# Optimization experiments

Hardware: AMD Instinct MI355X
Metric: run time of the kernel (lower is better)

The kernel has to match this reference:

```python
import jax, jax.numpy as jnp
import numpy as np

N_NODES = 100000
N_EDGES = 1600000
IN_DIM = 128
HID = 96
N_CLASSES = 16
BN_EPS = 1e-5
GIN_EPS = 0.0  # DGL GINConv default init_eps=0, learn_eps=False


def setup_inputs() -> dict:
    key = jax.random.key(0)
    ks = jax.random.split(key, 16)
    d = {}
    d["h"] = jax.random.normal(ks[0], (N_NODES, IN_DIM), dtype=jnp.float32)
    d["src"] = jax.random.randint(ks[1], (N_EDGES,), 0, N_NODES, dtype=jnp.int32)
    d["dst"] = jax.random.randint(ks[2], (N_EDGES,), 0, N_NODES, dtype=jnp.int32)
    # embedding_h: Linear(input_dim, hidden)
    d["W_emb"] = jax.random.normal(ks[3], (IN_DIM, HID), dtype=jnp.float32) / np.sqrt(IN_DIM)
    d["b_emb"] = jnp.zeros((HID,), dtype=jnp.float32)
    # GIN layer 1: MLP(1 layer) Linear(hid,hid) + BN(hid)
    d["W1"] = jax.random.normal(ks[4], (HID, HID), dtype=jnp.float32) / np.sqrt(HID)
    d["b1"] = jnp.zeros((HID,), dtype=jnp.float32)
    d["g1"] = jnp.ones((HID,), dtype=jnp.float32)
    d["be1"] = jnp.zeros((HID,), dtype=jnp.float32)
    # GIN layer 2
    d["W2"] = jax.random.normal(ks[5], (HID, HID), dtype=jnp.float32) / np.sqrt(HID)
    d["b2"] = jnp.zeros((HID,), dtype=jnp.float32)
    d["g2"] = jnp.ones((HID,), dtype=jnp.float32)
    d["be2"] = jnp.zeros((HID,), dtype=jnp.float32)
    # readout: Linear(hid, n_classes)
    d["Wr"] = jax.random.normal(ks[6], (HID, N_CLASSES), dtype=jnp.float32) / np.sqrt(HID)
    d["br"] = jnp.zeros((N_CLASSES,), dtype=jnp.float32)
    return d


def _gin_layer(h, src, dst, W, b, gamma, beta):
    # sum aggregation over incoming edges: agg[v] = sum_{(u,v) in E} h[u]
    agg = jax.ops.segment_sum(h[src], dst, num_segments=N_NODES)
    z = ((1.0 + GIN_EPS) * h + agg) @ W + b           # MLP (single linear)
    mu = jnp.mean(z, axis=0)                            # BatchNorm1d (batch stats)
    var = jnp.var(z, axis=0)
    z = (z - mu) * jax.lax.rsqrt(var + BN_EPS) * gamma + beta
    return jax.nn.relu(z)


def reference(h, src, dst, W_emb, b_emb, W1, b1, g1, be1, W2, b2, g2, be2, Wr, br):
    h = h @ W_emb + b_emb                               # embedding_h
    h = _gin_layer(h, src, dst, W1, b1, g1, be1)        # dropout treated as identity (eval)
    h = _gin_layer(h, src, dst, W2, b2, g2, be2)
    logits = h @ Wr + br                                # readout
    return jax.nn.log_softmax(logits, axis=1)
```

## Files before the change

### kernel.cpp

```cpp
#include <hip/hip_runtime.h>
#include <cmath>

#define N_NODES 100000
#define N_EDGES 1600000
#define IN_DIM 128
#define HID 96
#define NCLS 16
#define NB_GATH 2048

#define BSHIFT 7
#define BNODES 128
#define NBUK 782
#define TILE_E 8192
#define NBLK_E 196
#define NBLK_Q 24
#define NBLK_R 4

typedef unsigned int uint;
typedef unsigned short ushort;

__device__ __forceinline__ ushort f2bf(float x) {
    uint b = __float_as_uint(x);
    uint r = (b + 0x7FFFu + ((b >> 16) & 1u)) >> 16;
    return (ushort)r;
}
__device__ __forceinline__ float bf2f(ushort u) {
    return __uint_as_float(((uint)u) << 16);
}
__device__ __forceinline__ float bf_lo(uint w) { return __uint_as_float(w << 16); }
__device__ __forceinline__ float bf_hi(uint w) { return __uint_as_float(w & 0xFFFF0000u); }
__device__ __forceinline__ uint pack2bf(float a, float b) {
    return (uint)f2bf(a) | ((uint)f2bf(b) << 16);
}
__device__ __forceinline__ float4 bn_relu4(float4 x, float4 sc, float4 sh) {
    float4 r;
    r.x = fmaxf(fmaf(x.x, sc.x, sh.x), 0.f);
    r.y = fmaxf(fmaf(x.y, sc.y, sh.y), 0.f);
    r.z = fmaxf(fmaf(x.z, sc.z, sh.z), 0.f);
    r.w = fmaxf(fmaf(x.w, sc.w, sh.w), 0.f);
    return r;
}

__device__ __forceinline__ int tile_of(int blk) {
    int xcd = blk & 7, slot = blk >> 3;
    return (xcd < NBLK_R) ? xcd * (NBLK_Q + 1) + slot
                          : NBLK_R * (NBLK_Q + 1) + (xcd - NBLK_R) * NBLK_Q + slot;
}

__global__ __launch_bounds__(256) void wfuse(const float* __restrict__ W_emb,
                                             const float* __restrict__ W1,
                                             const float* __restrict__ b_emb,
                                             float* __restrict__ Wf,
                                             float* __restrict__ bf) {
    __shared__ float W1s[HID * HID];
    for (int i = threadIdx.x; i < HID * HID / 4; i += 256)
        ((float4*)W1s)[i] = ((const float4*)W1)[i];
    __syncthreads();
    int idx = blockIdx.x * 256 + threadIdx.x;
    if (idx < IN_DIM * HID) {
        int i = idx / HID, j = idx - (idx / HID) * HID;
        float acc = 0.f;
        for (int k = 0; k < HID; ++k)
            acc = fmaf(W_emb[(size_t)i * HID + k], W1s[k * HID + j], acc);
        Wf[idx] = acc;
    }
    if (idx < HID) {
        float acc = 0.f;
        for (int k = 0; k < HID; ++k)
            acc = fmaf(b_emb[k], W1s[k * HID + idx], acc);
        bf[idx] = acc;
    }
}

__global__ __launch_bounds__(192) void gemm_l1(const float* __restrict__ X,
                                               const float* __restrict__ W,
                                               const float* __restrict__ bias,
                                               ushort* __restrict__ outB) {
    constexpr int K = IN_DIM, KP = 64;
    constexpr int GSTRIDE = KP * 16 + 4;
    __shared__ float Ws[6 * GSTRIDE];
    __shared__ float bs[HID];
    if (threadIdx.x < HID) bs[threadIdx.x] = bias[threadIdx.x];

    const int g = threadIdx.x % 6;
    const int rc = threadIdx.x / 6;
    const int rbase = blockIdx.x * 64 + rc * 2;
    const int r0 = min(rbase + 0, N_NODES - 1);
    const int r1 = min(rbase + 1, N_NODES - 1);
    const float* x0 = X + (size_t)r0 * K;
    const float* x1 = X + (size_t)r1 * K;
    const float* wg = Ws + g * GSTRIDE;

    float acc[2][16];
#pragma unroll
    for (int j = 0; j < 16; ++j) { acc[0][j] = 0.f; acc[1][j] = 0.f; }

    for (int ph = 0; ph < K / KP; ++ph) {
        if (ph) __syncthreads();
        for (int i = threadIdx.x; i < KP * HID / 4; i += 192) {
            int flat = i * 4;
            int k = flat / HID, c = flat - k * HID;
            int gg = c / 16, j = c - gg * 16;
            *(float4*)&Ws[gg * GSTRIDE + k * 16 + j] =
                *(const float4*)(W + (size_t)(ph * KP + k) * HID + c);
        }
        __syncthreads();
        const float* xp0 = x0 + ph * KP;
        const float* xp1 = x1 + ph * KP;
        for (int k = 0; k < KP; k += 4) {
            float4 a0 = *(const float4*)(xp0 + k);
            float4 a1 = *(const float4*)(xp1 + k);
#pragma unroll
            for (int kk = 0; kk < 4; ++kk) {
                const float* wrow = wg + (k + kk) * 16;
                float4 w0 = *(const float4*)(wrow + 0);
                float4 w1 = *(const float4*)(wrow + 4);
                float4 w2 = *(const float4*)(wrow + 8);
                float4 w3 = *(const float4*)(wrow + 12);
                float xs0 = kk == 0 ? a0.x : kk == 1 ? a0.y : kk == 2 ? a0.z : a0.w;
                float xs1 = kk == 0 ? a1.x : kk == 1 ? a1.y : kk == 2 ? a1.z : a1.w;
                const float wv[16] = {w0.x, w0.y, w0.z, w0.w, w1.x, w1.y, w1.z, w1.w,
                                      w2.x, w2.y, w2.z, w2.w, w3.x, w3.y, w3.z, w3.w};
#pragma unroll
                for (int j = 0; j < 16; ++j) {
                    acc[0][j] = fmaf(xs0, wv[j], acc[0][j]);
                    acc[1][j] = fmaf(xs1, wv[j], acc[1][j]);
                }
            }
        }
    }
    const int rr[2] = {r0, r1};
#pragma unroll
    for (int i = 0; i < 2; ++i) {
        const float* bb = &bs[g * 16];
        ushort* orow = outB + (size_t)rr[i] * HID + g * 16;
        uint4 p0, p1;
        p0.x = pack2bf(acc[i][0] + bb[0], acc[i][1] + bb[1]);
        p0.y = pack2bf(acc[i][2] + bb[2], acc[i][3] + bb[3]);
        p0.z = pack2bf(acc[i][4] + bb[4], acc[i][5] + bb[5]);
        p0.w = pack2bf(acc[i][6] + bb[6], acc[i][7] + bb[7]);
        p1.x = pack2bf(acc[i][8] + bb[8], acc[i][9] + bb[9]);
        p1.y = pack2bf(acc[i][10] + bb[10], acc[i][11] + bb[11]);
        p1.z = pack2bf(acc[i][12] + bb[12], acc[i][13] + bb[13]);
        p1.w = pack2bf(acc[i][14] + bb[14], acc[i][15] + bb[15]);
        *(uint4*)(orow + 0) = p0;
        *(uint4*)(orow + 8) = p1;
    }
}

__global__ __launch_bounds__(192) void gemm_l2(const ushort* __restrict__ X,
                                               const float* __restrict__ W,
                                               const float* __restrict__ scale,
                                               const float* __restrict__ shift,
                                               ushort* __restrict__ outB) {
    constexpr int K = HID, KP = 48;
    constexpr int GSTRIDE = KP * 16 + 4;
    __shared__ float Ws[6 * GSTRIDE];
    __shared__ float scs[HID], shs[HID];
    if (threadIdx.x < HID) {
        scs[threadIdx.x] = scale[threadIdx.x];
        shs[threadIdx.x] = shift[threadIdx.x];
    }

    const int g = threadIdx.x % 6;
    const int rc = threadIdx.x / 6;
    const int rbase = blockIdx.x * 64 + rc * 2;
    const int r0 = min(rbase + 0, N_NODES - 1);
    const int r1 = min(rbase + 1, N_NODES - 1);
    const ushort* x0 = X + (size_t)r0 * K;
    const ushort* x1 = X + (size_t)r1 * K;
    const float* wg = Ws + g * GSTRIDE;

    float acc[2][16];
#pragma unroll
    for (int j = 0; j < 16; ++j) { acc[0][j] = 0.f; acc[1][j] = 0.f; }

    for (int ph = 0; ph < K / KP; ++ph) {
        if (ph) __syncthreads();
        for (int i = threadIdx.x; i < KP * HID / 4; i += 192) {
            int flat = i * 4;
            int k = flat / HID, c = flat - k * HID;
            int gg = c / 16, j = c - gg * 16;
            *(float4*)&Ws[gg * GSTRIDE + k * 16 + j] =
                *(const float4*)(W + (size_t)(ph * KP + k) * HID + c);
        }
        __syncthreads();
        const ushort* xp0 = x0 + ph * KP;
        const ushort* xp1 = x1 + ph * KP;
        for (int k = 0; k < KP; k += 4) {
            uint2 u0 = *(const uint2*)(xp0 + k);
            uint2 u1 = *(const uint2*)(xp1 + k);
            float4 sc4 = *(const float4*)(scs + ph * KP + k);
            float4 sh4 = *(const float4*)(shs + ph * KP + k);
            float4 a0 = bn_relu4(make_float4(bf_lo(u0.x), bf_hi(u0.x), bf_lo(u0.y), bf_hi(u0.y)), sc4, sh4);
            float4 a1 = bn_relu4(make_float4(bf_lo(u1.x), bf_hi(u1.x), bf_lo(u1.y), bf_hi(u1.y)), sc4, sh4);
#pragma unroll
            for (int kk = 0; kk < 4; ++kk) {
                const float* wrow = wg + (k + kk) * 16;
                float4 w0 = *(const float4*)(wrow + 0);
                float4 w1 = *(const float4*)(wrow + 4);
                float4 w2 = *(const float4*)(wrow + 8);
                float4 w3 = *(const float4*)(wrow + 12);
                float xs0 = kk == 0 ? a0.x : kk == 1 ? a0.y : kk == 2 ? a0.z : a0.w;
                float xs1 = kk == 0 ? a1.x : kk == 1 ? a1.y : kk == 2 ? a1.z : a1.w;
                const float wv[16] = {w0.x, w0.y, w0.z, w0.w, w1.x, w1.y, w1.z, w1.w,
                                      w2.x, w2.y, w2.z, w2.w, w3.x, w3.y, w3.z, w3.w};
#pragma unroll
                for (int j = 0; j < 16; ++j) {
                    acc[0][j] = fmaf(xs0, wv[j], acc[0][j]);
                    acc[1][j] = fmaf(xs1, wv[j], acc[1][j]);
                }
            }
        }
    }
    const int rr[2] = {r0, r1};
#pragma unroll
    for (int i = 0; i < 2; ++i) {
        ushort* orow = outB + (size_t)rr[i] * HID + g * 16;
        uint4 p0, p1;
        p0.x = pack2bf(acc[i][0], acc[i][1]);
        p0.y = pack2bf(acc[i][2], acc[i][3]);
        p0.z = pack2bf(acc[i][4], acc[i][5]);
        p0.w = pack2bf(acc[i][6], acc[i][7]);
        p1.x = pack2bf(acc[i][8], acc[i][9]);
        p1.y = pack2bf(acc[i][10], acc[i][11]);
        p1.z = pack2bf(acc[i][12], acc[i][13]);
        p1.w = pack2bf(acc[i][14], acc[i][15]);
        *(uint4*)(orow + 0) = p0;
        *(uint4*)(orow + 8) = p1;
    }
}

__global__ __launch_bounds__(256) void bin_hist(const int* __restrict__ dst,
                                                int* __restrict__ bcnt) {
    int tile = tile_of(blockIdx.x);
    int beg = tile * TILE_E, end = min(beg + TILE_E, N_EDGES);
    __shared__ int cnt[NBUK];
    for (int b = threadIdx.x; b < NBUK; b += 256) cnt[b] = 0;
    __syncthreads();
    for (int i = beg + threadIdx.x * 4; i < end; i += 256 * 4) {
        int4 d = *(const int4*)(dst + i);
        atomicAdd(&cnt[d.x >> BSHIFT], 1);
        atomicAdd(&cnt[d.y >> BSHIFT], 1);
        atomicAdd(&cnt[d.z >> BSHIFT], 1);
        atomicAdd(&cnt[d.w >> BSHIFT], 1);
    }
    __syncthreads();
    for (int b = threadIdx.x; b < NBUK; b += 256) bcnt[(size_t)b * NBLK_E + tile] = cnt[b];
}

__global__ __launch_bounds__(256) void bin_scanA(const int* __restrict__ bcnt,
                                                 int* __restrict__ boff,
                                                 int* __restrict__ btot) {
    int bin = blockIdx.x, t = threadIdx.x;
    __shared__ int tmp[256];
    int v = (t < NBLK_E) ? bcnt[(size_t)bin * NBLK_E + t] : 0;
    tmp[t] = v;
    __syncthreads();
    for (int off = 1; off < 256; off <<= 1) {
        int a = (t >= off) ? tmp[t - off] : 0;
        __syncthreads();
        tmp[t] += a;
        __syncthreads();
    }
    if (t < NBLK_E) boff[(size_t)bin * NBLK_E + t] = tmp[t] - v;
    if (t == NBLK_E - 1) btot[bin] = tmp[t];
}

__global__ __launch_bounds__(1024) void exscan782(const int* __restrict__ in,
                                                  int* __restrict__ out,
                                                  int sentinel) {
    int t = threadIdx.x;
    __shared__ int tmp[1024];
    int v = (t < NBUK) ? in[t] : 0;
    tmp[t] = v;
    __syncthreads();
    for (int off = 1; off < 1024; off <<= 1) {
        int a = (t >= off) ? tmp[t - off] : 0;
        __syncthreads();
        tmp[t] += a;
        __syncthreads();
    }
    if (t < NBUK) out[t] = tmp[t] - v;
    if (t == 0 && sentinel >= 0) out[NBUK] = sentinel;
}

__global__ __launch_bounds__(256) void bin_scatter(const int* __restrict__ src,
                                                   const int* __restrict__ dst,
                                                   const int* __restrict__ bbase,
                                                   const int* __restrict__ boff,
                                                   int* __restrict__ ebuf) {
    int tile = tile_of(blockIdx.x);
    int beg = tile * TILE_E, end = min(beg + TILE_E, N_EDGES);
    __shared__ int curs[NBUK];
    for (int b = threadIdx.x; b < NBUK; b += 256)
        curs[b] = bbase[b] + boff[(size_t)b * NBLK_E + tile];
    __syncthreads();
    for (int i = beg + threadIdx.x * 4; i < end; i += 256 * 4) {
        int4 d = *(const int4*)(dst + i);
        int4 s = *(const int4*)(src + i);
#pragma unroll
        for (int e = 0; e < 4; ++e) {
            int dv = e == 0 ? d.x : e == 1 ? d.y : e == 2 ? d.z : d.w;
            int sv = e == 0 ? s.x : e == 1 ? s.y : e == 2 ? s.z : s.w;
            int p = atomicAdd(&curs[dv >> BSHIFT], 1);
            ebuf[p] = (sv << BSHIFT) | (dv & (BNODES - 1));
        }
    }
}

__global__ __launch_bounds__(256) void bucket_hist(const int* __restrict__ ebuf,
                                                   const int* __restrict__ bbase,
                                                   int* __restrict__ deg,
                                                   int* __restrict__ bsumsB) {
    int b = blockIdx.x;
    int lo = b << BSHIFT;
    __shared__ int cnt[BNODES];
    if (threadIdx.x < BNODES) cnt[threadIdx.x] = 0;
    __syncthreads();
    int beg = bbase[b], end = bbase[b + 1];
    for (int i = beg + threadIdx.x; i < end; i += 256)
        atomicAdd(&cnt[ebuf[i] & (BNODES - 1)], 1);
    __syncthreads();
    if (threadIdx.x < BNODES && lo + threadIdx.x < N_NODES)
        deg[lo + threadIdx.x] = cnt[threadIdx.x];
    if (threadIdx.x < 64) cnt[threadIdx.x] += cnt[threadIdx.x + 64];
    __syncthreads();
    if (threadIdx.x < 32) cnt[threadIdx.x] += cnt[threadIdx.x + 32];
    __syncthreads();
    if (threadIdx.x < 16) cnt[threadIdx.x] += cnt[threadIdx.x + 16];
    __syncthreads();
    if (threadIdx.x == 0) {
        int s = 0;
        for (int i = 0; i < 16; ++i) s += cnt[i];
        bsumsB[b] = s;
    }
}

__global__ __launch_bounds__(128) void scan_final(const int* __restrict__ deg,
                                                  const int* __restrict__ boffs,
                                                  int* __restrict__ rp) {
    int b = blockIdx.x, t = threadIdx.x;
    int i = b * BNODES + t;
    int val = (i < N_NODES) ? deg[i] : 0;
    __shared__ int tmp[BNODES];
    tmp[t] = val;
    __syncthreads();
    for (int off = 1; off < BNODES; off <<= 1) {
        int a = (t >= off) ? tmp[t - off] : 0;
        __syncthreads();
        tmp[t] += a;
        __syncthreads();
    }
    int excl = tmp[t] - val + boffs[b];
    if (i < N_NODES) {
        rp[i] = excl;
        if (i == N_NODES - 1) rp[N_NODES] = excl + val;
    }
}

__global__ __launch_bounds__(256) void bucket_place(const int* __restrict__ ebuf,
                                                    const int* __restrict__ bbase,
                                                    const int* __restrict__ rp,
                                                    int* __restrict__ cols) {
    int b = blockIdx.x;
    int lo = b << BSHIFT;
    __shared__ int cur[BNODES];
    if (threadIdx.x < BNODES)
        cur[threadIdx.x] = (lo + threadIdx.x < N_NODES) ? rp[lo + threadIdx.x] : 0;
    __syncthreads();
    int beg = bbase[b], end = bbase[b + 1];
    for (int i = beg + threadIdx.x; i < end; i += 256) {
        int v = ebuf[i];
        int p = atomicAdd(&cur[v & (BNODES - 1)], 1);
        cols[p] = v >> BSHIFT;
    }
}

#define GLANES 24
#define GNODES 8

__global__ __launch_bounds__(192) void gather_stats(const ushort* __restrict__ T,
                                                    const int* __restrict__ rp,
                                                    const int* __restrict__ cols,
                                                    const float* __restrict__ bias,
                                                    ushort* __restrict__ z,
                                                    float* __restrict__ psums,
                                                    float* __restrict__ psq) {
    const int q = threadIdx.x % GLANES;
    const int rs = threadIdx.x / GLANES;
    const float4 bias4 = ((const float4*)bias)[q];
    float4 s = make_float4(0.f, 0.f, 0.f, 0.f);
    float4 sq = make_float4(0.f, 0.f, 0.f, 0.f);

#define ADDROW(u)                                                              \
    {                                                                          \
        ushort4 w = *(const ushort4*)(T + (size_t)(u) * HID + q * 4);          \
        a.x += bf2f(w.x); a.y += bf2f(w.y);                                    \
        a.z += bf2f(w.z); a.w += bf2f(w.w);                                    \
    }

    for (int v = blockIdx.x * GNODES + rs; v < N_NODES; v += NB_GATH * GNODES) {
        float4 a = bias4;
        ADDROW(v);
        int beg = rp[v], end = rp[v + 1];
        int j = beg;
        for (; j + 3 < end; j += 4) {
            int u0 = cols[j], u1 = cols[j + 1], u2 = cols[j + 2], u3 = cols[j + 3];
            ADDROW(u0); ADDROW(u1); ADDROW(u2); ADDROW(u3);
        }
        for (; j < end; ++j) ADDROW(cols[j]);

        uint2 o;
        o.x = pack2bf(a.x, a.y);
        o.y = pack2bf(a.z, a.w);
        *(uint2*)(z + (size_t)v * HID + q * 4) = o;
        s.x += a.x; s.y += a.y; s.z += a.z; s.w += a.w;
        sq.x = fmaf(a.x, a.x, sq.x);
        sq.y = fmaf(a.y, a.y, sq.y);
        sq.z = fmaf(a.z, a.z, sq.z);
        sq.w = fmaf(a.w, a.w, sq.w);
    }
#undef ADDROW

    __shared__ float4 ls[GNODES][GLANES], lq[GNODES][GLANES];
    ls[rs][q] = s;
    lq[rs][q] = sq;
    __syncthreads();
    if (threadIdx.x < GLANES) {
        float4 S = ls[0][threadIdx.x], Q = lq[0][threadIdx.x];
#pragma unroll
        for (int i = 1; i < GNODES; ++i) {
            S.x += ls[i][threadIdx.x].x; S.y += ls[i][threadIdx.x].y;
            S.z += ls[i][threadIdx.x].z; S.w += ls[i][threadIdx.x].w;
            Q.x += lq[i][threadIdx.x].x; Q.y += lq[i][threadIdx.x].y;
            Q.z += lq[i][threadIdx.x].z; Q.w += lq[i][threadIdx.x].w;
        }
        ((float4*)(psums + (size_t)blockIdx.x * HID))[threadIdx.x] = S;
        ((float4*)(psq + (size_t)blockIdx.x * HID))[threadIdx.x] = Q;
    }
}

__global__ __launch_bounds__(384) void bn_finalize(const float* __restrict__ psums,
                                                   const float* __restrict__ psq,
                                                   const float* __restrict__ g,
                                                   const float* __restrict__ be,
                                                   float* __restrict__ scale,
                                                   float* __restrict__ shift) {
    int c = threadIdx.x % 96, h = threadIdx.x / 96;
    float S = 0.f, Q = 0.f;
    for (int b = h * (NB_GATH / 4); b < (h + 1) * (NB_GATH / 4); ++b) {
        S += psums[(size_t)b * HID + c];
        Q += psq[(size_t)b * HID + c];
    }
    __shared__ float lS[4][96], lQ[4][96];
    lS[h][c] = S;
    lQ[h][c] = Q;
    __syncthreads();
    if (threadIdx.x < 96) {
        S = lS[0][c] + lS[1][c] + lS[2][c] + lS[3][c];
        Q = lQ[0][c] + lQ[1][c] + lQ[2][c] + lQ[3][c];
        float mu = S * (1.0f / N_NODES);
        float var = Q * (1.0f / N_NODES) - mu * mu;
        float rstd = rsqrtf(var + 1e-5f);
        float sc = g[c] * rstd;
        scale[c] = sc;
        shift[c] = be[c] - mu * sc;
    }
}

__global__ __launch_bounds__(256) void readout_kernel(const ushort* __restrict__ X,
                                                      const float* __restrict__ scale,
                                                      const float* __restrict__ shift,
                                                      const float* __restrict__ Wr,
                                                      const float* __restrict__ br,
                                                      float* __restrict__ out) {
    __shared__ float Ws[HID * NCLS];
    __shared__ float XL[16 * 97];
    __shared__ float scs[HID], shs[HID], bs[NCLS];
    for (int i = threadIdx.x; i < HID * NCLS / 4; i += 256)
        ((float4*)Ws)[i] = ((const float4*)Wr)[i];
    if (threadIdx.x < HID) {
        scs[threadIdx.x] = scale[threadIdx.x];
        shs[threadIdx.x] = shift[threadIdx.x];
    }
    if (threadIdx.x < NCLS) bs[threadIdx.x] = br[threadIdx.x];

    int rr = threadIdx.x >> 4, t = threadIdx.x & 15;
    for (int tile = blockIdx.x; tile < N_NODES / 16; tile += gridDim.x) {
        int rbase = tile * 16;
        __syncthreads();
        if (threadIdx.x < 192) {
            int base = threadIdx.x * 8;
            int row = base / HID, col = base - (base / HID) * HID;
            uint4 w = *(const uint4*)(X + (size_t)rbase * HID + base);
            float v[8] = {bf_lo(w.x), bf_hi(w.x), bf_lo(w.y), bf_hi(w.y),
                          bf_lo(w.z), bf_hi(w.z), bf_lo(w.w), bf_hi(w.w)};
#pragma unroll
            for (int e = 0; e < 8; ++e)
                XL[row * 97 + col + e] = fmaxf(fmaf(v[e], scs[col + e], shs[col + e]), 0.f);
        }
        __syncthreads();
        float acc = bs[t];
        const float* xrow = &XL[rr * 97];
#pragma unroll 4
        for (int k = 0; k < HID; ++k) acc = fmaf(xrow[k], Ws[k * NCLS + t], acc);
        float m = acc;
#pragma unroll
        for (int off = 8; off; off >>= 1) m = fmaxf(m, __shfl_xor(m, off, 16));
        float e = expf(acc - m);
        float sum = e;
#pragma unroll
        for (int off = 8; off; off >>= 1) sum += __shfl_xor(sum, off, 16);
        float lse = m + logf(sum);
        out[(size_t)rbase * NCLS + threadIdx.x] = acc - lse;
    }
}

extern "C" void kernel_launch(void* const* d_in, const int* in_sizes, int n_in,
                              void* d_out, int out_size, void* d_ws, size_t ws_size,
                              hipStream_t stream) {
    const float* h     = (const float*)d_in[0];
    const int*   src   = (const int*)d_in[1];
    const int*   dst   = (const int*)d_in[2];
    const float* W_emb = (const float*)d_in[3];
    const float* b_emb = (const float*)d_in[4];
    const float* W1    = (const float*)d_in[5];
    const float* b1    = (const float*)d_in[6];
    const float* g1    = (const float*)d_in[7];
    const float* be1   = (const float*)d_in[8];
    const float* W2    = (const float*)d_in[9];
    const float* b2    = (const float*)d_in[10];
    const float* g2    = (const float*)d_in[11];
    const float* be2   = (const float*)d_in[12];
    const float* Wr    = (const float*)d_in[13];
    const float* br    = (const float*)d_in[14];

    const size_t nh = (size_t)N_NODES * HID;
    ushort* z    = (ushort*)d_ws;
    ushort* T    = z + nh;
    int* deg     = (int*)(T + nh);
    int* rp      = deg + N_NODES;
    int* cols    = rp + N_NODES + 1;
    int* ebuf    = cols + N_EDGES;
    int* bcnt    = ebuf + N_EDGES;
    int* boff    = bcnt + NBUK * NBLK_E;
    int* btot    = boff + NBUK * NBLK_E;
    int* bbase   = btot + NBUK;
    int* bsumsB  = bbase + NBUK + 1;
    int* boffs   = bsumsB + NBUK;
    float* psums = (float*)(boffs + NBUK);
    float* psq   = psums + (size_t)NB_GATH * HID;
    float* scale = psq + (size_t)NB_GATH * HID;
    float* shift = scale + HID;
    float* Wf    = shift + HID;
    float* bf    = Wf + IN_DIM * HID;

    const int blkT = (N_NODES + 63) / 64;

    bin_hist<<<NBLK_E, 256, 0, stream>>>(dst, bcnt);
    bin_scanA<<<NBUK, 256, 0, stream>>>(bcnt, boff, btot);
    exscan782<<<1, 1024, 0, stream>>>(btot, bbase, N_EDGES);
    bin_scatter<<<NBLK_E, 256, 0, stream>>>(src, dst, bbase, boff, ebuf);
    bucket_hist<<<NBUK, 256, 0, stream>>>(ebuf, bbase, deg, bsumsB);
    exscan782<<<1, 1024, 0, stream>>>(bsumsB, boffs, -1);
    scan_final<<<NBUK, 128, 0, stream>>>(deg, boffs, rp);
    bucket_place<<<NBUK, 256, 0, stream>>>(ebuf, bbase, rp, cols);
    wfuse<<<(IN_DIM * HID + 255) / 256, 256, 0, stream>>>(W_emb, W1, b_emb, Wf, bf);

    gemm_l1<<<blkT, 192, 0, stream>>>(h, Wf, bf, T);
    gather_stats<<<NB_GATH, 192, 0, stream>>>(T, rp, cols, b1, z, psums, psq);
    bn_finalize<<<1, 384, 0, stream>>>(psums, psq, g1, be1, scale, shift);

    gemm_l2<<<blkT, 192, 0, stream>>>(z, W2, scale, shift, T);
    gather_stats<<<NB_GATH, 192, 0, stream>>>(T, rp, cols, b2, z, psums, psq);
    bn_finalize<<<1, 384, 0, stream>>>(psums, psq, g2, be2, scale, shift);

    readout_kernel<<<2048, 256, 0, stream>>>(z, scale, shift, Wr, br, (float*)d_out);
}
```

Before: 378.4 us.

## Replace FP32 FMA GEMMs with bf16 MFMA 16x16x32 tiles in both layers

Both dense node-feature GEMMs now stage a 96-row input tile and a transposed bf16 copy of the weight matrix in shared memory. The products run on MFMA bf16 matrix instructions, with six waves each computing 16 rows by 96 columns, replacing the scalar FP32 FMA loops. Inputs and weights are rounded to bf16 before the multiply, which adds precision loss on top of the existing bf16 outputs. Each block also re-converts the whole weight matrix with scalar strided loads, and the output stores are scattered 2-byte writes rather than vectorised ones.

```diff
diff --git a/kernel.cpp b/kernel.cpp
--- a/kernel.cpp
+++ b/kernel.cpp
@@ -18,6 +18,8 @@
 
 typedef unsigned int uint;
 typedef unsigned short ushort;
+typedef __attribute__((ext_vector_type(8))) short short8v;
+typedef __attribute__((ext_vector_type(4))) float float4v;
 
 __device__ __forceinline__ ushort f2bf(float x) {
     uint b = __float_as_uint(x);
@@ -31,14 +33,6 @@
 __device__ __forceinline__ float bf_hi(uint w) { return __uint_as_float(w & 0xFFFF0000u); }
 __device__ __forceinline__ uint pack2bf(float a, float b) {
     return (uint)f2bf(a) | ((uint)f2bf(b) << 16);
-}
-__device__ __forceinline__ float4 bn_relu4(float4 x, float4 sc, float4 sh) {
-    float4 r;
-    r.x = fmaxf(fmaf(x.x, sc.x, sh.x), 0.f);
-    r.y = fmaxf(fmaf(x.y, sc.y, sh.y), 0.f);
-    r.z = fmaxf(fmaf(x.z, sc.z, sh.z), 0.f);
-    r.w = fmaxf(fmaf(x.w, sc.w, sh.w), 0.f);
-    return r;
 }
 
 __device__ __forceinline__ int tile_of(int blk) {
@@ -72,162 +66,129 @@
     }
 }
 
-__global__ __launch_bounds__(192) void gemm_l1(const float* __restrict__ X,
+__global__ __launch_bounds__(384) void gemm_l1(const float* __restrict__ X,
                                                const float* __restrict__ W,
                                                const float* __restrict__ bias,
                                                ushort* __restrict__ outB) {
-    constexpr int K = IN_DIM, KP = 64;
-    constexpr int GSTRIDE = KP * 16 + 4;
-    __shared__ float Ws[6 * GSTRIDE];
+    constexpr int K = IN_DIM, KPAD = K + 8;
+    __shared__ ushort A_s[96 * KPAD];
+    __shared__ ushort W_t[96 * KPAD];
     __shared__ float bs[HID];
     if (threadIdx.x < HID) bs[threadIdx.x] = bias[threadIdx.x];
 
-    const int g = threadIdx.x % 6;
-    const int rc = threadIdx.x / 6;
-    const int rbase = blockIdx.x * 64 + rc * 2;
-    const int r0 = min(rbase + 0, N_NODES - 1);
-    const int r1 = min(rbase + 1, N_NODES - 1);
-    const float* x0 = X + (size_t)r0 * K;
-    const float* x1 = X + (size_t)r1 * K;
-    const float* wg = Ws + g * GSTRIDE;
-
-    float acc[2][16];
-#pragma unroll
-    for (int j = 0; j < 16; ++j) { acc[0][j] = 0.f; acc[1][j] = 0.f; }
-
-    for (int ph = 0; ph < K / KP; ++ph) {
-        if (ph) __syncthreads();
-        for (int i = threadIdx.x; i < KP * HID / 4; i += 192) {
-            int flat = i * 4;
-            int k = flat / HID, c = flat - k * HID;
-            int gg = c / 16, j = c - gg * 16;
-            *(float4*)&Ws[gg * GSTRIDE + k * 16 + j] =
-                *(const float4*)(W + (size_t)(ph * KP + k) * HID + c);
-        }
-        __syncthreads();
-        const float* xp0 = x0 + ph * KP;
-        const float* xp1 = x1 + ph * KP;
-        for (int k = 0; k < KP; k += 4) {
-            float4 a0 = *(const float4*)(xp0 + k);
-            float4 a1 = *(const float4*)(xp1 + k);
-#pragma unroll
-            for (int kk = 0; kk < 4; ++kk) {
-                const float* wrow = wg + (k + kk) * 16;
-                float4 w0 = *(const float4*)(wrow + 0);
-                float4 w1 = *(const float4*)(wrow + 4);
-                float4 w2 = *(const float4*)(wrow + 8);
-                float4 w3 = *(const float4*)(wrow + 12);
-                float xs0 = kk == 0 ? a0.x : kk == 1 ? a0.y : kk == 2 ? a0.z : a0.w;
-                float xs1 = kk == 0 ? a1.x : kk == 1 ? a1.y : kk == 2 ? a1.z : a1.w;
-                const float wv[16] = {w0.x, w0.y, w0.z, w0.w, w1.x, w1.y, w1.z, w1.w,
-                                      w2.x, w2.y, w2.z, w2.w, w3.x, w3.y, w3.z, w3.w};
-#pragma unroll
-                for (int j = 0; j < 16; ++j) {
-                    acc[0][j] = fmaf(xs0, wv[j], acc[0][j]);
-                    acc[1][j] = fmaf(xs1, wv[j], acc[1][j]);
-                }
-            }
-        }
-    }
-    const int rr[2] = {r0, r1};
-#pragma unroll
-    for (int i = 0; i < 2; ++i) {
-        const float* bb = &bs[g * 16];
-        ushort* orow = outB + (size_t)rr[i] * HID + g * 16;
-        uint4 p0, p1;
-        p0.x = pack2bf(acc[i][0] + bb[0], acc[i][1] + bb[1]);
-        p0.y = pack2bf(acc[i][2] + bb[2], acc[i][3] + bb[3]);
-        p0.z = pack2bf(acc[i][4] + bb[4], acc[i][5] + bb[5]);
-        p0.w = pack2bf(acc[i][6] + bb[6], acc[i][7] + bb[7]);
-        p1.x = pack2bf(acc[i][8] + bb[8], acc[i][9] + bb[9]);
-        p1.y = pack2bf(acc[i][10] + bb[10], acc[i][11] + bb[11]);
-        p1.z = pack2bf(acc[i][12] + bb[12], acc[i][13] + bb[13]);
-        p1.w = pack2bf(acc[i][14] + bb[14], acc[i][15] + bb[15]);
-        *(uint4*)(orow + 0) = p0;
-        *(uint4*)(orow + 8) = p1;
-    }
-}
-
-__global__ __launch_bounds__(192) void gemm_l2(const ushort* __restrict__ X,
+    const int rbase = blockIdx.x * 96;
+    for (int c = threadIdx.x; c < 96 * (K / 8); c += 384) {
+        int row = c / (K / 8), ko = (c - row * (K / 8)) * 8;
+        int gr = min(rbase + row, N_NODES - 1);
+        const float* xp = X + (size_t)gr * K + ko;
+        float4 v0 = *(const float4*)xp;
+        float4 v1 = *(const float4*)(xp + 4);
+        uint4 p;
+        p.x = pack2bf(v0.x, v0.y);
+        p.y = pack2bf(v0.z, v0.w);
+        p.z = pack2bf(v1.x, v1.y);
+        p.w = pack2bf(v1.z, v1.w);
+        *(uint4*)&A_s[row * KPAD + ko] = p;
+    }
+    for (int j = threadIdx.x; j < K * HID; j += 384) {
+        int k = j / HID, n = j - k * HID;
+        W_t[n * KPAD + k] = f2bf(W[j]);
+    }
+    __syncthreads();
+
+    const int lane = threadIdx.x & 63, w = threadIdx.x >> 6;
+    const int ar = lane & 15, kg = lane >> 4;
+    float4v acc[6] = {};
+    const ushort* ap = &A_s[(w * 16 + ar) * KPAD + kg * 8];
+    const ushort* bp = &W_t[ar * KPAD + kg * 8];
+#pragma unroll
+    for (int kc = 0; kc < K / 32; ++kc) {
+        short8v af = *(const short8v*)(ap + kc * 32);
+#pragma unroll
+        for (int ct = 0; ct < 6; ++ct) {
+            short8v bfv = *(const short8v*)(bp + ct * 16 * KPAD + kc * 32);
+            acc[ct] = __builtin_amdgcn_mfma_f32_16x16x32_bf16(af, bfv, acc[ct], 0, 0, 0);
+        }
+    }
+#pragma unroll
+    for (int ct = 0; ct < 6; ++ct) {
+        int col = ct * 16 + ar;
+        float bb = bs[col];
+#pragma unroll
+        for (int i = 0; i < 4; ++i) {
+            int grow = rbase + w * 16 + kg * 4 + i;
+            if (grow < N_NODES)
+                outB[(size_t)grow * HID + col] = f2bf(acc[ct][i] + bb);
+        }
+    }
+}
+
+__global__ __launch_bounds__(384) void gemm_l2(const ushort* __restrict__ X,
                                                const float* __restrict__ W,
                                                const float* __restrict__ scale,
                                                const float* __restrict__ shift,
                                                ushort* __restrict__ outB) {
-    constexpr int K = HID, KP = 48;
-    constexpr int GSTRIDE = KP * 16 + 4;
-    __shared__ float Ws[6 * GSTRIDE];
+    constexpr int K = HID, KPAD = K + 8;
+    __shared__ ushort A_s[96 * KPAD];
+    __shared__ ushort W_t[96 * KPAD];
     __shared__ float scs[HID], shs[HID];
     if (threadIdx.x < HID) {
         scs[threadIdx.x] = scale[threadIdx.x];
         shs[threadIdx.x] = shift[threadIdx.x];
     }
-
-    const int g = threadIdx.x % 6;
-    const int rc = threadIdx.x / 6;
-    const int rbase = blockIdx.x * 64 + rc * 2;
-    const int r0 = min(rbase + 0, N_NODES - 1);
-    const int r1 = min(rbase + 1, N_NODES - 1);
-    const ushort* x0 = X + (size_t)r0 * K;
-    const ushort* x1 = X + (size_t)r1 * K;
-    const float* wg = Ws + g * GSTRIDE;
-
-    float acc[2][16];
-#pragma unroll
-    for (int j = 0; j < 16; ++j) { acc[0][j] = 0.f; acc[1][j] = 0.f; }
-
-    for (int ph = 0; ph < K / KP; ++ph) {
-        if (ph) __syncthreads();
-        for (int i = threadIdx.x; i < KP * HID / 4; i += 192) {
-            int flat = i * 4;
-            int k = flat / HID, c = flat - k * HID;
-            int gg = c / 16, j = c - gg * 16;
-            *(float4*)&Ws[gg * GSTRIDE + k * 16 + j] =
-                *(const float4*)(W + (size_t)(ph * KP + k) * HID + c);
-        }
-        __syncthreads();
-        const ushort* xp0 = x0 + ph * KP;
-        const ushort* xp1 = x1 + ph * KP;
-        for (int k = 0; k < KP; k += 4) {
-            uint2 u0 = *(const uint2*)(xp0 + k);
-            uint2 u1 = *(const uint2*)(xp1 + k);
-            float4 sc4 = *(const float4*)(scs + ph * KP + k);
-            float4 sh4 = *(const float4*)(shs + ph * KP + k);
-            float4 a0 = bn_relu4(make_float4(bf_lo(u0.x), bf_hi(u0.x), bf_lo(u0.y), bf_hi(u0.y)), sc4, sh4);
-            float4 a1 = bn_relu4(make_float4(bf_lo(u1.x), bf_hi(u1.x), bf_lo(u1.y), bf_hi(u1.y)), sc4, sh4);
-#pragma unroll
-            for (int kk = 0; kk < 4; ++kk) {
-                const float* wrow = wg + (k + kk) * 16;
-                float4 w0 = *(const float4*)(wrow + 0);
-                float4 w1 = *(const float4*)(wrow + 4);
-                float4 w2 = *(const float4*)(wrow + 8);
-                float4 w3 = *(const float4*)(wrow + 12);
-                float xs0 = kk == 0 ? a0.x : kk == 1 ? a0.y : kk == 2 ? a0.z : a0.w;
-                float xs1 = kk == 0 ? a1.x : kk == 1 ? a1.y : kk == 2 ? a1.z : a1.w;
-                const float wv[16] = {w0.x, w0.y, w0.z, w0.w, w1.x, w1.y, w1.z, w1.w,
-                                      w2.x, w2.y, w2.z, w2.w, w3.x, w3.y, w3.z, w3.w};
-#pragma unroll
-                for (int j = 0; j < 16; ++j) {
-                    acc[0][j] = fmaf(xs0, wv[j], acc[0][j]);
-                    acc[1][j] = fmaf(xs1, wv[j], acc[1][j]);
-                }
-            }
-        }
-    }
-    const int rr[2] = {r0, r1};
-#pragma unroll
-    for (int i = 0; i < 2; ++i) {
-        ushort* orow = outB + (size_t)rr[i] * HID + g * 16;
-        uint4 p0, p1;
-        p0.x = pack2bf(acc[i][0], acc[i][1]);
-        p0.y = pack2bf(acc[i][2], acc[i][3]);
-        p0.z = pack2bf(acc[i][4], acc[i][5]);
-        p0.w = pack2bf(acc[i][6], acc[i][7]);
-        p1.x = pack2bf(acc[i][8], acc[i][9]);
-        p1.y = pack2bf(acc[i][10], acc[i][11]);
-        p1.z = pack2bf(acc[i][12], acc[i][13]);
-        p1.w = pack2bf(acc[i][14], acc[i][15]);
-        *(uint4*)(orow + 0) = p0;
-        *(uint4*)(orow + 8) = p1;
+    __syncthreads();
+
+    const int rbase = blockIdx.x * 96;
+    for (int c = threadIdx.x; c < 96 * (K / 8); c += 384) {
+        int row = c / (K / 8), ko = (c - row * (K / 8)) * 8;
+        int gr = min(rbase + row, N_NODES - 1);
+        uint4 u = *(const uint4*)(X + (size_t)gr * K + ko);
+        float4 sA = *(const float4*)&scs[ko], sB = *(const float4*)&scs[ko + 4];
+        float4 hA = *(const float4*)&shs[ko], hB = *(const float4*)&shs[ko + 4];
+        float v0 = fmaxf(fmaf(bf_lo(u.x), sA.x, hA.x), 0.f);
+        float v1 = fmaxf(fmaf(bf_hi(u.x), sA.y, hA.y), 0.f);
+        float v2 = fmaxf(fmaf(bf_lo(u.y), sA.z, hA.z), 0.f);
+        float v3 = fmaxf(fmaf(bf_hi(u.y), sA.w, hA.w), 0.f);
+        float v4 = fmaxf(fmaf(bf_lo(u.z), sB.x, hB.x), 0.f);
+        float v5 = fmaxf(fmaf(bf_hi(u.z), sB.y, hB.y), 0.f);
+        float v6 = fmaxf(fmaf(bf_lo(u.w), sB.z, hB.z), 0.f);
+        float v7 = fmaxf(fmaf(bf_hi(u.w), sB.w, hB.w), 0.f);
+        uint4 p;
+        p.x = pack2bf(v0, v1);
+        p.y = pack2bf(v2, v3);
+        p.z = pack2bf(v4, v5);
+        p.w = pack2bf(v6, v7);
+        *(uint4*)&A_s[row * KPAD + ko] = p;
+    }
+    for (int j = threadIdx.x; j < K * HID; j += 384) {
+        int k = j / HID, n = j - k * HID;
+        W_t[n * KPAD + k] = f2bf(W[j]);
+    }
+    __syncthreads();
+
+    const int lane = threadIdx.x & 63, w = threadIdx.x >> 6;
+    const int ar = lane & 15, kg = lane >> 4;
+    float4v acc[6] = {};
+    const ushort* ap = &A_s[(w * 16 + ar) * KPAD + kg * 8];
+    const ushort* bp = &W_t[ar * KPAD + kg * 8];
+#pragma unroll
+    for (int kc = 0; kc < K / 32; ++kc) {
+        short8v af = *(const short8v*)(ap + kc * 32);
+#pragma unroll
+        for (int ct = 0; ct < 6; ++ct) {
+            short8v bfv = *(const short8v*)(bp + ct * 16 * KPAD + kc * 32);
+            acc[ct] = __builtin_amdgcn_mfma_f32_16x16x32_bf16(af, bfv, acc[ct], 0, 0, 0);
+        }
+    }
+#pragma unroll
+    for (int ct = 0; ct < 6; ++ct) {
+        int col = ct * 16 + ar;
+#pragma unroll
+        for (int i = 0; i < 4; ++i) {
+            int grow = rbase + w * 16 + kg * 4 + i;
+            if (grow < N_NODES)
+                outB[(size_t)grow * HID + col] = f2bf(acc[ct][i]);
+        }
     }
 }
 
@@ -556,7 +517,7 @@
     float* Wf    = shift + HID;
     float* bf    = Wf + IN_DIM * HID;
 
-    const int blkT = (N_NODES + 63) / 64;
+    const int blkT = (N_NODES + 95) / 96;
 
     bin_hist<<<NBLK_E, 256, 0, stream>>>(dst, bcnt);
     bin_scanA<<<NBUK, 256, 0, stream>>>(bcnt, boff, btot);
@@ -568,11 +529,11 @@
     bucket_place<<<NBUK, 256, 0, stream>>>(ebuf, bbase, rp, cols);
     wfuse<<<(IN_DIM * HID + 255) / 256, 256, 0, stream>>>(W_emb, W1, b_emb, Wf, bf);
 
-    gemm_l1<<<blkT, 192, 0, stream>>>(h, Wf, bf, T);
+    gemm_l1<<<blkT, 384, 0, stream>>>(h, Wf, bf, T);
     gather_stats<<<NB_GATH, 192, 0, stream>>>(T, rp, cols, b1, z, psums, psq);
     bn_finalize<<<1, 384, 0, stream>>>(psums, psq, g1, be1, scale, shift);
 
-    gemm_l2<<<blkT, 192, 0, stream>>>(z, W2, scale, shift, T);
+    gemm_l2<<<blkT, 384, 0, stream>>>(z, W2, scale, shift, T);
     gather_stats<<<NB_GATH, 192, 0, stream>>>(T, rp, cols, b2, z, psums, psq);
     bn_finalize<<<1, 384, 0, stream>>>(psums, psq, g2, be2, scale, shift);
 
```

Result: faster. 323.4 us (-14.6%).
